# Optimization experiments

Hardware: AMD Instinct MI355X
Metric: run time of the kernel (lower is better)

## Reference

```python
import jax, jax.numpy as jnp
import numpy as np

B, O, H, I = 256, 128, 1024, 2048  # batch, objects, hidden, input_size
Hh = H // 2  # 512; x_j feature dim
DF = I - Hh  # 1536; X_F feature dim


def _xavier(key, shape):
    fan_in, fan_out = shape[1], shape[0]
    lim = np.sqrt(6.0 / (fan_in + fan_out))
    return jax.random.uniform(key, shape, jnp.float32, -lim, lim)


def setup_inputs() -> dict:
    key = jax.random.key(0)
    ks = jax.random.split(key, 24)
    mask = jax.random.bernoulli(ks[0], 0.7, (B, O))
    mask = mask.at[:, 0].set(True)  # ensure at least one valid object per row
    inp = {
        "x_j": jax.random.normal(ks[1], (B, O, Hh), jnp.float32),
        "x_mask": mask,
        "X_F": jax.random.normal(ks[2], (B, DF), jnp.float32),
        "h": jax.random.normal(ks[3], (B, 1, H), jnp.float32),
        "c": jax.random.normal(ks[4], (B, 1, H), jnp.float32),
    }
    names_W = ["W_i", "W_f", "W_c", "W_o"]
    names_U = ["U_i", "U_f", "U_c", "U_o"]
    names_V = ["V_i", "V_f", "V_c", "V_o"]
    k = 5
    for n in names_W:
        inp[n] = _xavier(ks[k], (H, I)); k += 1
    for n in names_U + names_V:
        inp[n] = _xavier(ks[k], (H, H)); k += 1
    for n in ["b_i", "b_f", "b_c", "b_o"]:
        inp[n] = jnp.zeros((H,), jnp.float32)
    inp["w"] = _xavier(ks[k], (1, Hh)); k += 1
    inp["W_e"] = _xavier(ks[k], (Hh, H)); k += 1
    inp["U_e"] = _xavier(ks[k], (Hh, Hh)); k += 1
    inp["b_e"] = jnp.zeros((Hh,), jnp.float32)
    return inp


def reference(x_j, x_mask, X_F, h, c,
              W_i, W_f, W_c, W_o,
              U_i, U_f, U_c, U_o,
              V_i, V_f, V_c, V_o,
              b_i, b_f, b_c, b_o,
              w, W_e, U_e, b_e):
    # Additive attention over objects.
    # h: (B,1,H) -> (B,1,Hh) broadcasts against x_j proj (B,O,Hh)
    e = jnp.tanh(h @ W_e.T + x_j @ U_e.T + b_e)      # (B,O,Hh)
    e = (e @ w.T)[..., 0]                              # (B,O)
    e = jnp.where(x_mask, e, -1e9)
    a = jax.nn.softmax(e, axis=1)                      # (B,O)
    phi_j = jnp.einsum('bo,bok->bk', a, x_j)[:, None, :]  # (B,1,Hh)
    x = jnp.concatenate([phi_j, X_F[:, None, :]], axis=2)  # (B,1,I)

    # Peephole LSTM gates (h, c: (B,1,H))
    i = jax.nn.sigmoid(x @ W_i.T + h @ U_i.T + c @ V_i.T + b_i)
    f = jax.nn.sigmoid(x @ W_f.T + h @ U_f.T + c @ V_f.T + b_f)
    new_c = f * c + i * jnp.tanh(x @ W_c.T + h @ U_c.T + b_c)
    o = jax.nn.sigmoid(x @ W_o.T + h @ U_o.T + c @ V_o.T + b_o)
    new_h = o * jnp.tanh(new_c)
    return new_h, new_c
```

## Files before the change

kernel.cpp:

```cpp
#include <hip/hip_runtime.h>
#include <hip/hip_bf16.h>

typedef unsigned char u8;
typedef unsigned short u16;
typedef unsigned int u32;
typedef __attribute__((ext_vector_type(8))) short bf8;
typedef __attribute__((ext_vector_type(4))) float f4;

#define B_ 256
#define O_ 128
#define Hh_ 512
#define H_ 1024
#define DF_ 1536
#define I_ 2048

#define HWE_OFF   0
#define XC_OFF    524288
#define PRE_OFF   2621440
#define FLAG_OFF  6815744
#define XJ16_OFF  7340032
#define UE16_OFF  40894464
#define WS_BIG    41418752
#define GPART_OFF XJ16_OFF

__device__ __forceinline__ float bflo(u32 u){ union{u32 i; float f;} v; v.i = u<<16; return v.f; }
__device__ __forceinline__ float bfhi(u32 u){ union{u32 i; float f;} v; v.i = u & 0xffff0000u; return v.f; }
__device__ __forceinline__ float bf1(u16 u){ union{u32 i; float f;} v; v.i = ((u32)u)<<16; return v.f; }
__device__ __forceinline__ u16 f2bf(float f){
    __hip_bfloat16 h = __float2bfloat16(f);
    union{ __hip_bfloat16 h; u16 u; } v; v.h = h; return v.u;
}
__device__ __forceinline__ u32 pack2(float a, float b){
    return ((u32)f2bf(a)) | (((u32)f2bf(b))<<16);
}
struct P8 { uint4 lo, hi; };
__device__ __forceinline__ P8 fetch8(const void* p, size_t idx, int isf32){
    P8 r;
    if(isf32){
        const uint4* f = (const uint4*)((const float*)p + idx);
        r.lo = f[0]; r.hi = f[1];
    } else {
        r.lo = *(const uint4*)((const u16*)p + idx);
    }
    return r;
}
__device__ __forceinline__ uint4 cvt8(P8 r, int isf32){
    if(isf32){
        float4 x = *(float4*)&r.lo, y = *(float4*)&r.hi;
        uint4 o;
        o.x = pack2(x.x,x.y); o.y = pack2(x.z,x.w);
        o.z = pack2(y.x,y.y); o.w = pack2(y.z,y.w);
        return o;
    }
    return r.lo;
}
__device__ __forceinline__ uint4 load8(const void* p, size_t idx, int isf32){
    return cvt8(fetch8(p, idx, isf32), isf32);
}
__device__ __forceinline__ float loads(const void* p, size_t idx, int isf32){
    return isf32 ? ((const float*)p)[idx] : bf1(((const u16*)p)[idx]);
}
__device__ __forceinline__ float fast_tanh(float x){
    return 1.0f - 2.0f/(__expf(2.0f*x)+1.0f);
}
__device__ __forceinline__ float sigmoidf_(float x){
    return 1.0f/(1.0f+__expf(-x));
}

__global__ void k_detect(const u8* __restrict__ m, const u16* __restrict__ xj,
                         int* __restrict__ flags){
    __shared__ int n1, n2, n3, mb, xo;
    int t = threadIdx.x;
    if(t==0){ n1=0; n2=0; n3=0; mb=0; xo=0; }
    __syncthreads();
    int a1=0, a2=0, a3=0, amax=0;
    for(int i=t; i<8192; i+=256){
        int v = m[i]; int c = i&3;
        if(c==1) a1|=v;
        if(c==2) a2|=v;
        if(c==3) a3|=v;
        amax = amax > v ? amax : v;
    }
    if(a1) atomicOr(&n1,1);
    if(a2) atomicOr(&n2,1);
    if(a3) atomicOr(&n3,1);
    atomicMax(&mb, amax);
    int e = 0;
    for(int i=t; i<2048; i+=256){
        u32 u = xj[2*i];
        int ex = (u>>7)&0xFF;
        if(ex >= 156) e = 1;
    }
    if(e) atomicOr(&xo,1);
    __syncthreads();
    if(t==0){
        int w;
        if(!n1 && !n2 && !n3)      w = 4;
        else if(!n1 && n2 && n3)   w = 4;
        else if(mb > 1)            w = 2;
        else                       w = 1;
        flags[0] = w;
        flags[1] = xo;
    }
}

__global__ __launch_bounds__(256) void k_conv(const void* __restrict__ xj,
                                              const void* __restrict__ Ue,
                                              const int* __restrict__ flags,
                                              u16* __restrict__ xj16,
                                              u16* __restrict__ ue16){
    int isf32 = flags[1];
    size_t g = (size_t)blockIdx.x*256 + threadIdx.x;
    if(g < 2097152){
        size_t idx = g*8;
        *(uint4*)&xj16[idx] = load8(xj, idx, isf32);
    } else {
        size_t idx = (g - 2097152)*8;
        *(uint4*)&ue16[idx] = load8(Ue, idx, isf32);
    }
}

__global__ __launch_bounds__(256) void k_hwe(const void* __restrict__ h,
                                             const void* __restrict__ We,
                                             const int* __restrict__ flags,
                                             float* __restrict__ hwe){
    int n0 = blockIdx.x*64;
    int kc = blockIdx.y*128;
    int m0 = blockIdx.z*128;
    int t = threadIdx.x;
    int isf32 = flags[1];
    __shared__ __align__(16) u16 As[128*40];
    __shared__ __align__(16) u16 Bs[64*40];
    int w = t>>6, lane = t&63;
    int q = lane>>4, l16 = lane&15;
    int koff = q*8;
    f4 acc[2][4];
    for(int mi=0;mi<2;mi++) for(int ni=0;ni<4;ni++){
        f4 z = {0.f,0.f,0.f,0.f}; acc[mi][ni] = z;
    }
    for(int ks=0; ks<128; ks+=32){
        __syncthreads();
        for(int i=0;i<2;i++){
            int row = i*64 + (t>>2), cv = t&3;
            uint4 va = load8(h, (size_t)(m0+row)*H_ + kc + ks + cv*8, isf32);
            *(uint4*)&As[row*40 + cv*8] = va;
        }
        {
            int row = t>>2, cv = t&3;
            uint4 vb = load8(We, (size_t)(n0+row)*H_ + kc + ks + cv*8, isf32);
            *(uint4*)&Bs[row*40 + cv*8] = vb;
        }
        __syncthreads();
        bf8 af[2], bfr[4];
        for(int mi=0;mi<2;mi++) af[mi]  = *(const bf8*)&As[(w*32+mi*16+l16)*40 + koff];
        for(int ni=0;ni<4;ni++) bfr[ni] = *(const bf8*)&Bs[(ni*16+l16)*40 + koff];
        for(int mi=0;mi<2;mi++)
            for(int ni=0;ni<4;ni++)
                acc[mi][ni] = __builtin_amdgcn_mfma_f32_16x16x32_bf16(af[mi], bfr[ni], acc[mi][ni], 0,0,0);
    }
    for(int mi=0;mi<2;mi++){
        for(int r=0;r<4;r++){
            int brow = m0 + w*32 + mi*16 + q*4 + r;
            for(int ni=0;ni<4;ni++){
                int ncol = n0 + ni*16 + l16;
                atomicAdd(&hwe[(size_t)brow*Hh_ + ncol], acc[mi][ni][r]);
            }
        }
    }
}

__global__ __launch_bounds__(256) void k_pack(const void* __restrict__ XF,
                                              const void* __restrict__ h,
                                              const void* __restrict__ c,
                                              const int* __restrict__ flags,
                                              u16* __restrict__ Xc){
    int b = blockIdx.y;
    int r = blockIdx.x*256 + threadIdx.x;
    int isf32 = flags[1];
    float v;
    if(r < DF_)            v = loads(XF, (size_t)b*DF_ + r, isf32);
    else if(r < DF_ + H_)  v = loads(h,  (size_t)b*H_ + (r - DF_), isf32);
    else                   v = loads(c,  (size_t)b*H_ + (r - DF_ - H_), isf32);
    Xc[(size_t)b*4096 + 512 + r] = f2bf(v);
}

__global__ __launch_bounds__(256) void k_attn(const void* __restrict__ xjA,
                                              const void* __restrict__ wvec,
                                              const void* __restrict__ UeA,
                                              const void* __restrict__ be,
                                              const float* __restrict__ hwe,
                                              const int* __restrict__ flags,
                                              int srcbf,
                                              float* __restrict__ Epart){
    int b = blockIdx.x, nc = blockIdx.y, t = threadIdx.x;
    int isf = flags[1];
    int isA = srcbf ? 0 : isf;
    __shared__ __align__(16) u16 As[128*40];
    __shared__ __align__(16) u16 Bs[64*40];
    __shared__ float hwes[64];
    __shared__ float wvs[64];

    if(t < 64){
        int col = nc*64 + t;
        hwes[t] = hwe[(size_t)b*Hh_ + col] + loads(be, col, isf);
        wvs[t]  = loads(wvec, col, isf);
    }

    const size_t xboff = (size_t)b*O_*Hh_;
    int w = t>>6, lane = t&63;
    int q = lane>>4, l16 = lane&15;
    int koff = q*8;
    int rA = t>>2, cA = t&3;

    f4 acc[2][4];
    for(int mi=0;mi<2;mi++) for(int ni=0;ni<4;ni++){
        f4 z = {0.f,0.f,0.f,0.f}; acc[mi][ni] = z;
    }

    P8 pa0, pa1, pb;
    pa0 = fetch8(xjA, xboff + (size_t)rA*Hh_      + cA*8, isA);
    pa1 = fetch8(xjA, xboff + (size_t)(rA+64)*Hh_ + cA*8, isA);
    pb  = fetch8(UeA, (size_t)(nc*64 + rA)*Hh_    + cA*8, isA);

    for(int ks=0; ks<Hh_; ks+=32){
        __syncthreads();
        *(uint4*)&As[rA*40 + cA*8]      = cvt8(pa0, isA);
        *(uint4*)&As[(rA+64)*40 + cA*8] = cvt8(pa1, isA);
        *(uint4*)&Bs[rA*40 + cA*8]      = cvt8(pb, isA);
        __syncthreads();
        if(ks + 32 < Hh_){
            int kn = ks + 32;
            pa0 = fetch8(xjA, xboff + (size_t)rA*Hh_      + kn + cA*8, isA);
            pa1 = fetch8(xjA, xboff + (size_t)(rA+64)*Hh_ + kn + cA*8, isA);
            pb  = fetch8(UeA, (size_t)(nc*64 + rA)*Hh_    + kn + cA*8, isA);
        }
        bf8 af[2], bfr[4];
        for(int mi=0;mi<2;mi++) af[mi]  = *(const bf8*)&As[(w*32+mi*16+l16)*40 + koff];
        for(int ni=0;ni<4;ni++) bfr[ni] = *(const bf8*)&Bs[(ni*16+l16)*40 + koff];
        for(int mi=0;mi<2;mi++)
            for(int ni=0;ni<4;ni++)
                acc[mi][ni] = __builtin_amdgcn_mfma_f32_16x16x32_bf16(af[mi], bfr[ni], acc[mi][ni], 0,0,0);
    }
    for(int mi=0;mi<2;mi++){
        for(int r=0;r<4;r++){
            int o = w*32 + mi*16 + q*4 + r;
            float part = 0.f;
            for(int ni=0;ni<4;ni++){
                int col = ni*16 + l16;
                part += wvs[col] * fast_tanh(hwes[col] + acc[mi][ni][r]);
            }
            part += __shfl_xor(part, 1);
            part += __shfl_xor(part, 2);
            part += __shfl_xor(part, 4);
            part += __shfl_xor(part, 8);
            if(l16 == 0) Epart[(size_t)nc*32768 + (size_t)b*O_ + o] = part;
        }
    }
}

__global__ __launch_bounds__(512) void k_soft(const float* __restrict__ Epart,
                                              const void* __restrict__ maskp,
                                              const void* __restrict__ xjA,
                                              const int* __restrict__ flags,
                                              int srcbf,
                                              u16* __restrict__ Xc){
    int b = blockIdx.x, t = threadIdx.x;
    int isf = flags[1];
    int isA = srcbf ? 0 : isf;
    int mw = flags[0];
    __shared__ float es[O_];
    __shared__ float as_[O_];
    __shared__ float red[2];
    if(t < O_){
        float e = 0.f;
        for(int p=0;p<8;p++) e += Epart[(size_t)p*32768 + (size_t)b*O_ + t];
        size_t mi_ = (size_t)b*O_ + t;
        bool valid;
        if(mw == 1)      valid = ((const u8*)maskp)[mi_]  != 0;
        else if(mw == 2) valid = ((const u16*)maskp)[mi_] != 0;
        else             valid = ((const u32*)maskp)[mi_] != 0;
        es[t] = valid ? e : -1e30f;
    }
    __syncthreads();
    if(t < 64){
        float v = fmaxf(es[t], es[t+64]);
        for(int m=32;m>0;m>>=1) v = fmaxf(v, __shfl_xor(v, m));
        if(t==0) red[0] = v;
    }
    __syncthreads();
    if(t < O_) as_[t] = __expf(es[t] - red[0]);
    __syncthreads();
    if(t < 64){
        float v = as_[t] + as_[t+64];
        for(int m=32;m>0;m>>=1) v += __shfl_xor(v, m);
        if(t==0) red[1] = v;
    }
    __syncthreads();
    float inv = 1.0f / red[1];
    float acc = 0.f;
    size_t base = (size_t)b*O_*Hh_ + t;
    #pragma unroll 8
    for(int o=0;o<O_;o++){
        acc += as_[o] * loads(xjA, base + (size_t)o*Hh_, isA);
    }
    Xc[(size_t)b*4096 + t] = f2bf(acc * inv);
}

__global__ __launch_bounds__(512) void k_gates(const u16* __restrict__ Xc,
    const void* __restrict__ Wi, const void* __restrict__ Wf, const void* __restrict__ Wc, const void* __restrict__ Wo,
    const void* __restrict__ Ui, const void* __restrict__ Uf, const void* __restrict__ Uc, const void* __restrict__ Uo,
    const void* __restrict__ Vi, const void* __restrict__ Vf, const void* __restrict__ Vo,
    const int* __restrict__ flags,
    int dosplit,
    float* __restrict__ part){
    int nt = blockIdx.x;
    int kc = blockIdx.y;
    int g  = nt>>4;
    int k0 = kc*512;
    if(g == 2 && k0 >= 3072) return;
    int isf32 = flags[1];
    const void* Wm = (g==0)?Wi:(g==1)?Wf:(g==2)?Wc:Wo;
    const void* Um = (g==0)?Ui:(g==1)?Uf:(g==2)?Uc:Uo;
    const void* Vm = (g==0)?Vi:(g==1)?Vf:(g==3)?Vo:Vi;
    int n0 = (nt&15)*64;
    int t = threadIdx.x;
    __shared__ __align__(16) u16 As[256*40];
    __shared__ __align__(16) u16 Bs[64*40];
    int w = t>>6, lane = t&63;
    int q = lane>>4, l16 = lane&15;
    int koff = q*8;
    int rA = t>>2, cA = t&3;
    bool hasB = (t < 256);

    f4 acc[2][4];
    for(int mi=0;mi<2;mi++) for(int ni=0;ni<4;ni++){
        f4 z = {0.f,0.f,0.f,0.f}; acc[mi][ni] = z;
    }

    auto fetchB = [&](int k)->P8{
        int n = n0 + rA;
        if(k < 2048)       return fetch8(Wm, (size_t)n*I_ + k, isf32);
        else if(k < 3072)  return fetch8(Um, (size_t)n*H_ + (k-2048), isf32);
        else               return fetch8(Vm, (size_t)n*H_ + (k-3072), isf32);
    };

    uint4 qa0, qa1; P8 qb;
    qa0 = *(const uint4*)(Xc + (size_t)rA*4096       + k0 + cA*8);
    qa1 = *(const uint4*)(Xc + (size_t)(rA+128)*4096 + k0 + cA*8);
    if(hasB) qb = fetchB(k0 + cA*8);

    for(int ks=0; ks<512; ks+=32){
        __syncthreads();
        *(uint4*)&As[rA*40 + cA*8]       = qa0;
        *(uint4*)&As[(rA+128)*40 + cA*8] = qa1;
        if(hasB) *(uint4*)&Bs[rA*40 + cA*8] = cvt8(qb, isf32);
        __syncthreads();
        if(ks + 32 < 512){
            int kn = k0 + ks + 32;
            qa0 = *(const uint4*)(Xc + (size_t)rA*4096       + kn + cA*8);
            qa1 = *(const uint4*)(Xc + (size_t)(rA+128)*4096 + kn + cA*8);
            if(hasB) qb = fetchB(kn + cA*8);
        }
        bf8 af[2], bfr[4];
        for(int mi=0;mi<2;mi++) af[mi]  = *(const bf8*)&As[(w*32+mi*16+l16)*40 + koff];
        for(int ni=0;ni<4;ni++) bfr[ni] = *(const bf8*)&Bs[(ni*16+l16)*40 + koff];
        for(int mi=0;mi<2;mi++)
            for(int ni=0;ni<4;ni++)
                acc[mi][ni] = __builtin_amdgcn_mfma_f32_16x16x32_bf16(af[mi], bfr[ni], acc[mi][ni], 0,0,0);
    }
    float* pg = dosplit ? (part + ((size_t)kc*4 + g)*(size_t)(B_*H_))
                        : (part + (size_t)g*(B_*H_));
    for(int mi=0;mi<2;mi++){
        for(int r=0;r<4;r++){
            int brow = w*32 + mi*16 + q*4 + r;
            for(int ni=0;ni<4;ni++){
                int ncol = n0 + ni*16 + l16;
                size_t o = (size_t)brow*H_ + ncol;
                if(dosplit) pg[o] = acc[mi][ni][r];
                else        atomicAdd(&pg[o], acc[mi][ni][r]);
            }
        }
    }
}

__global__ __launch_bounds__(256) void k_combine(const float* __restrict__ part,
    int nsplit, int climit,
    const void* __restrict__ c,
    const void* __restrict__ bi, const void* __restrict__ bfv,
    const void* __restrict__ bc, const void* __restrict__ bo,
    const int* __restrict__ flags,
    float* __restrict__ out){
    int b = blockIdx.x, t = threadIdx.x;
    int isf32 = flags[1];
    const size_t G = (size_t)B_*H_;
    for(int i=0;i<4;i++){
        int n = i*256 + t;
        size_t idx = (size_t)b*H_ + n;
        float pi = 0.f, pf = 0.f, pcv = 0.f, po = 0.f;
        for(int p=0;p<nsplit;p++){
            const float* pp = part + (size_t)p*4*G;
            pi += pp[idx];
            pf += pp[G + idx];
            po += pp[3*G + idx];
            if(p < climit) pcv += pp[2*G + idx];
        }
        pi  += loads(bi,  n, isf32);
        pf  += loads(bfv, n, isf32);
        pcv += loads(bc,  n, isf32);
        po  += loads(bo,  n, isf32);
        float ig = sigmoidf_(pi);
        float fg = sigmoidf_(pf);
        float og = sigmoidf_(po);
        float cold = loads(c, idx, isf32);
        float ncv = fg*cold + ig*fast_tanh(pcv);
        float nh  = og*fast_tanh(ncv);
        out[idx]     = nh;
        out[G + idx] = ncv;
    }
}

extern "C" void kernel_launch(void* const* d_in, const int* in_sizes, int n_in,
                              void* d_out, int out_size, void* d_ws, size_t ws_size,
                              hipStream_t stream){
    const void* xj   = d_in[0];
    const void* mask = d_in[1];
    const void* XF   = d_in[2];
    const void* h    = d_in[3];
    const void* c    = d_in[4];
    const void* Wi   = d_in[5];
    const void* Wf   = d_in[6];
    const void* Wc   = d_in[7];
    const void* Wo   = d_in[8];
    const void* Ui   = d_in[9];
    const void* Uf   = d_in[10];
    const void* Uc   = d_in[11];
    const void* Uo   = d_in[12];
    const void* Vi   = d_in[13];
    const void* Vf   = d_in[14];
    const void* Vo   = d_in[16];
    const void* bi   = d_in[17];
    const void* bfv  = d_in[18];
    const void* bc   = d_in[19];
    const void* bo   = d_in[20];
    const void* wv   = d_in[21];
    const void* We   = d_in[22];
    const void* Ue   = d_in[23];
    const void* be   = d_in[24];

    char* ws = (char*)d_ws;
    float* hwe  = (float*)(ws + HWE_OFF);
    u16*   Xc   = (u16*)(ws + XC_OFF);
    float* pre  = (float*)(ws + PRE_OFF);
    int*   flags= (int*)(ws + FLAG_OFF);
    float* out  = (float*)d_out;

    int big = (ws_size >= (size_t)WS_BIG);
    u16* xj16 = (u16*)(ws + XJ16_OFF);
    u16* ue16 = (u16*)(ws + UE16_OFF);
    float* gpart = (float*)(ws + GPART_OFF);
    const void* xjA = big ? (const void*)xj16 : xj;
    const void* UeA = big ? (const void*)ue16 : Ue;

    k_detect<<<1, 256, 0, stream>>>((const u8*)mask, (const u16*)xj, flags);
    hipMemsetAsync(hwe, 0, (size_t)B_*Hh_*sizeof(float), stream);
    if(big) k_conv<<<8320, 256, 0, stream>>>(xj, Ue, flags, xj16, ue16);
    k_hwe<<<dim3(8,8,2), 256, 0, stream>>>(h, We, flags, hwe);
    k_pack<<<dim3(14, B_), 256, 0, stream>>>(XF, h, c, flags, Xc);
    k_attn<<<dim3(B_, 8), 256, 0, stream>>>(xjA, wv, UeA, be, hwe, flags, big, pre);
    k_soft<<<B_, 512, 0, stream>>>(pre, mask, xjA, flags, big, Xc);
    if(big){
        k_gates<<<dim3(64, 8), 512, 0, stream>>>(Xc, Wi,Wf,Wc,Wo, Ui,Uf,Uc,Uo, Vi,Vf,Vo, flags, 1, gpart);
        k_combine<<<B_, 256, 0, stream>>>(gpart, 8, 6, c, bi, bfv, bc, bo, flags, out);
    } else {
        hipMemsetAsync(pre, 0, (size_t)4*B_*H_*sizeof(float), stream);
        k_gates<<<dim3(64, 8), 512, 0, stream>>>(Xc, Wi,Wf,Wc,Wo, Ui,Uf,Uc,Uo, Vi,Vf,Vo, flags, 0, pre);
        k_combine<<<B_, 256, 0, stream>>>(pre, 1, 1, c, bi, bfv, bc, bo, flags, out);
    }
}
```

Measured before the change: 337.9 us.

## Fuse attention scoring and softmax per batch, drop x_j bf16 conversion pass

Attention projection, tanh-score reduction and softmax/weighted sum are merged into one kernel per batch row. Each wave keeps its x_j A-fragments in registers and loops over all 512 columns of U_e, so the separate x_j-to-bf16 conversion kernel and the Epart round trip are gone. The h·W_e partial sums are now written to separate split buffers instead of atomics, which removes a memset. The gates GEMM K-step also grows from 32 to 64 with wider LDS tiles. The cost is that parallelism for the attention stage drops to 256 blocks, and register pressure rises from the 16 held A fragments and 16 accumulators.

```diff
diff --git a/kernel.cpp b/kernel.cpp
--- a/kernel.cpp
+++ b/kernel.cpp
@@ -23,8 +23,6 @@
 #define WS_BIG    41418752
 #define GPART_OFF XJ16_OFF
 
-__device__ __forceinline__ float bflo(u32 u){ union{u32 i; float f;} v; v.i = u<<16; return v.f; }
-__device__ __forceinline__ float bfhi(u32 u){ union{u32 i; float f;} v; v.i = u & 0xffff0000u; return v.f; }
 __device__ __forceinline__ float bf1(u16 u){ union{u32 i; float f;} v; v.i = ((u32)u)<<16; return v.f; }
 __device__ __forceinline__ u16 f2bf(float f){
     __hip_bfloat16 h = __float2bfloat16(f);
@@ -104,26 +102,19 @@
     }
 }
 
-__global__ __launch_bounds__(256) void k_conv(const void* __restrict__ xj,
-                                              const void* __restrict__ Ue,
-                                              const int* __restrict__ flags,
-                                              u16* __restrict__ xj16,
-                                              u16* __restrict__ ue16){
+__global__ __launch_bounds__(256) void k_conv_ue(const void* __restrict__ Ue,
+                                                 const int* __restrict__ flags,
+                                                 u16* __restrict__ ue16){
     int isf32 = flags[1];
     size_t g = (size_t)blockIdx.x*256 + threadIdx.x;
-    if(g < 2097152){
-        size_t idx = g*8;
-        *(uint4*)&xj16[idx] = load8(xj, idx, isf32);
-    } else {
-        size_t idx = (g - 2097152)*8;
-        *(uint4*)&ue16[idx] = load8(Ue, idx, isf32);
-    }
+    size_t idx = g*8;
+    *(uint4*)&ue16[idx] = load8(Ue, idx, isf32);
 }
 
 __global__ __launch_bounds__(256) void k_hwe(const void* __restrict__ h,
                                              const void* __restrict__ We,
                                              const int* __restrict__ flags,
-                                             float* __restrict__ hwe){
+                                             float* __restrict__ hwePart){
     int n0 = blockIdx.x*64;
     int kc = blockIdx.y*128;
     int m0 = blockIdx.z*128;
@@ -158,12 +149,13 @@
             for(int ni=0;ni<4;ni++)
                 acc[mi][ni] = __builtin_amdgcn_mfma_f32_16x16x32_bf16(af[mi], bfr[ni], acc[mi][ni], 0,0,0);
     }
+    float* hp = hwePart + (size_t)blockIdx.y*(B_*Hh_);
     for(int mi=0;mi<2;mi++){
         for(int r=0;r<4;r++){
             int brow = m0 + w*32 + mi*16 + q*4 + r;
             for(int ni=0;ni<4;ni++){
                 int ncol = n0 + ni*16 + l16;
-                atomicAdd(&hwe[(size_t)brow*Hh_ + ncol], acc[mi][ni][r]);
+                hp[(size_t)brow*Hh_ + ncol] = acc[mi][ni][r];
             }
         }
     }
@@ -184,102 +176,101 @@
     Xc[(size_t)b*4096 + 512 + r] = f2bf(v);
 }
 
-__global__ __launch_bounds__(256) void k_attn(const void* __restrict__ xjA,
-                                              const void* __restrict__ wvec,
-                                              const void* __restrict__ UeA,
-                                              const void* __restrict__ be,
-                                              const float* __restrict__ hwe,
-                                              const int* __restrict__ flags,
-                                              int srcbf,
-                                              float* __restrict__ Epart){
-    int b = blockIdx.x, nc = blockIdx.y, t = threadIdx.x;
-    int isf = flags[1];
-    int isA = srcbf ? 0 : isf;
-    __shared__ __align__(16) u16 As[128*40];
-    __shared__ __align__(16) u16 Bs[64*40];
-    __shared__ float hwes[64];
-    __shared__ float wvs[64];
-
-    if(t < 64){
-        int col = nc*64 + t;
-        hwes[t] = hwe[(size_t)b*Hh_ + col] + loads(be, col, isf);
-        wvs[t]  = loads(wvec, col, isf);
-    }
-
-    const size_t xboff = (size_t)b*O_*Hh_;
-    int w = t>>6, lane = t&63;
-    int q = lane>>4, l16 = lane&15;
-    int koff = q*8;
-    int rA = t>>2, cA = t&3;
-
-    f4 acc[2][4];
-    for(int mi=0;mi<2;mi++) for(int ni=0;ni<4;ni++){
-        f4 z = {0.f,0.f,0.f,0.f}; acc[mi][ni] = z;
-    }
-
-    P8 pa0, pa1, pb;
-    pa0 = fetch8(xjA, xboff + (size_t)rA*Hh_      + cA*8, isA);
-    pa1 = fetch8(xjA, xboff + (size_t)(rA+64)*Hh_ + cA*8, isA);
-    pb  = fetch8(UeA, (size_t)(nc*64 + rA)*Hh_    + cA*8, isA);
-
-    for(int ks=0; ks<Hh_; ks+=32){
-        __syncthreads();
-        *(uint4*)&As[rA*40 + cA*8]      = cvt8(pa0, isA);
-        *(uint4*)&As[(rA+64)*40 + cA*8] = cvt8(pa1, isA);
-        *(uint4*)&Bs[rA*40 + cA*8]      = cvt8(pb, isA);
-        __syncthreads();
-        if(ks + 32 < Hh_){
-            int kn = ks + 32;
-            pa0 = fetch8(xjA, xboff + (size_t)rA*Hh_      + kn + cA*8, isA);
-            pa1 = fetch8(xjA, xboff + (size_t)(rA+64)*Hh_ + kn + cA*8, isA);
-            pb  = fetch8(UeA, (size_t)(nc*64 + rA)*Hh_    + kn + cA*8, isA);
-        }
-        bf8 af[2], bfr[4];
-        for(int mi=0;mi<2;mi++) af[mi]  = *(const bf8*)&As[(w*32+mi*16+l16)*40 + koff];
-        for(int ni=0;ni<4;ni++) bfr[ni] = *(const bf8*)&Bs[(ni*16+l16)*40 + koff];
-        for(int mi=0;mi<2;mi++)
-            for(int ni=0;ni<4;ni++)
-                acc[mi][ni] = __builtin_amdgcn_mfma_f32_16x16x32_bf16(af[mi], bfr[ni], acc[mi][ni], 0,0,0);
-    }
-    for(int mi=0;mi<2;mi++){
-        for(int r=0;r<4;r++){
-            int o = w*32 + mi*16 + q*4 + r;
-            float part = 0.f;
-            for(int ni=0;ni<4;ni++){
-                int col = ni*16 + l16;
-                part += wvs[col] * fast_tanh(hwes[col] + acc[mi][ni][r]);
-            }
-            part += __shfl_xor(part, 1);
-            part += __shfl_xor(part, 2);
-            part += __shfl_xor(part, 4);
-            part += __shfl_xor(part, 8);
-            if(l16 == 0) Epart[(size_t)nc*32768 + (size_t)b*O_ + o] = part;
-        }
-    }
-}
-
-__global__ __launch_bounds__(512) void k_soft(const float* __restrict__ Epart,
-                                              const void* __restrict__ maskp,
-                                              const void* __restrict__ xjA,
-                                              const int* __restrict__ flags,
-                                              int srcbf,
-                                              u16* __restrict__ Xc){
+__global__ __launch_bounds__(512) void k_attn_fused(const void* __restrict__ xj,
+                                                    const void* __restrict__ UeB,
+                                                    const void* __restrict__ wvec,
+                                                    const void* __restrict__ be,
+                                                    const float* __restrict__ hwePart,
+                                                    const void* __restrict__ maskp,
+                                                    const int* __restrict__ flags,
+                                                    int ueIsBf,
+                                                    u16* __restrict__ Xc){
     int b = blockIdx.x, t = threadIdx.x;
     int isf = flags[1];
-    int isA = srcbf ? 0 : isf;
+    int isB = ueIsBf ? 0 : isf;
     int mw = flags[0];
+    __shared__ __align__(16) u16 Bs[256*72];
+    __shared__ float hwes[512];
+    __shared__ float wvs[512];
     __shared__ float es[O_];
     __shared__ float as_[O_];
     __shared__ float red[2];
+    __shared__ int msk[O_];
+
+    int w = t>>6, l = t&63, l16 = l&15, q = l>>4;
+    int m0 = w*16;
+
+    {
+        float s = 0.f;
+        #pragma unroll
+        for(int p=0;p<8;p++) s += hwePart[(size_t)p*(B_*Hh_) + (size_t)b*Hh_ + t];
+        hwes[t] = s + loads(be, t, isf);
+        wvs[t]  = loads(wvec, t, isf);
+    }
     if(t < O_){
-        float e = 0.f;
-        for(int p=0;p<8;p++) e += Epart[(size_t)p*32768 + (size_t)b*O_ + t];
         size_t mi_ = (size_t)b*O_ + t;
         bool valid;
         if(mw == 1)      valid = ((const u8*)maskp)[mi_]  != 0;
         else if(mw == 2) valid = ((const u16*)maskp)[mi_] != 0;
         else             valid = ((const u32*)maskp)[mi_] != 0;
-        es[t] = valid ? e : -1e30f;
+        msk[t] = valid ? 1 : 0;
+    }
+
+    bf8 afr[16];
+    const size_t arow = ((size_t)b*O_ + m0 + l16)*Hh_;
+    #pragma unroll
+    for(int kt=0;kt<16;kt++){
+        P8 p = fetch8(xj, arow + kt*32 + q*8, isf);
+        uint4 u = cvt8(p, isf);
+        afr[kt] = *(bf8*)&u;
+    }
+
+    float ep[4] = {0.f,0.f,0.f,0.f};
+    #pragma unroll
+    for(int hh=0; hh<2; hh++){
+        int nbase = hh*256;
+        f4 acc[16];
+        #pragma unroll
+        for(int ni=0;ni<16;ni++){ f4 z={0.f,0.f,0.f,0.f}; acc[ni]=z; }
+        #pragma unroll
+        for(int ks=0;ks<8;ks++){
+            __syncthreads();
+            #pragma unroll
+            for(int j=0;j<4;j++){
+                int slot = t + j*512;
+                int row = slot>>3, cv = slot&7;
+                P8 p = fetch8(UeB, (size_t)(nbase+row)*Hh_ + ks*64 + cv*8, isB);
+                *(uint4*)&Bs[row*72 + cv*8] = cvt8(p, isB);
+            }
+            __syncthreads();
+            #pragma unroll
+            for(int ni=0;ni<16;ni++){
+                #pragma unroll
+                for(int kk=0;kk<2;kk++){
+                    bf8 bfrag = *(const bf8*)&Bs[(ni*16+l16)*72 + kk*32 + q*8];
+                    acc[ni] = __builtin_amdgcn_mfma_f32_16x16x32_bf16(afr[ks*2+kk], bfrag, acc[ni], 0,0,0);
+                }
+            }
+        }
+        #pragma unroll
+        for(int ni=0;ni<16;ni++){
+            int col = nbase + ni*16 + l16;
+            float wv = wvs[col], hw = hwes[col];
+            #pragma unroll
+            for(int r=0;r<4;r++) ep[r] += wv * fast_tanh(hw + acc[ni][r]);
+        }
+    }
+    #pragma unroll
+    for(int r=0;r<4;r++){
+        float v = ep[r];
+        v += __shfl_xor(v, 1);
+        v += __shfl_xor(v, 2);
+        v += __shfl_xor(v, 4);
+        v += __shfl_xor(v, 8);
+        if(l16 == 0){
+            int o = m0 + q*4 + r;
+            es[o] = msk[o] ? v : -1e30f;
+        }
     }
     __syncthreads();
     if(t < 64){
@@ -297,13 +288,13 @@
     }
     __syncthreads();
     float inv = 1.0f / red[1];
-    float acc = 0.f;
+    float acc2 = 0.f;
     size_t base = (size_t)b*O_*Hh_ + t;
     #pragma unroll 8
     for(int o=0;o<O_;o++){
-        acc += as_[o] * loads(xjA, base + (size_t)o*Hh_, isA);
-    }
-    Xc[(size_t)b*4096 + t] = f2bf(acc * inv);
+        acc2 += as_[o] * loads(xj, base + (size_t)o*Hh_, isf);
+    }
+    Xc[(size_t)b*4096 + t] = f2bf(acc2 * inv);
 }
 
 __global__ __launch_bounds__(512) void k_gates(const u16* __restrict__ Xc,
@@ -324,49 +315,65 @@
     const void* Vm = (g==0)?Vi:(g==1)?Vf:(g==3)?Vo:Vi;
     int n0 = (nt&15)*64;
     int t = threadIdx.x;
-    __shared__ __align__(16) u16 As[256*40];
-    __shared__ __align__(16) u16 Bs[64*40];
+    __shared__ __align__(16) u16 As[256*72];
+    __shared__ __align__(16) u16 Bs[64*72];
     int w = t>>6, lane = t&63;
     int q = lane>>4, l16 = lane&15;
-    int koff = q*8;
-    int rA = t>>2, cA = t&3;
-    bool hasB = (t < 256);
+    int rB = t>>3, cB = t&7;
 
     f4 acc[2][4];
     for(int mi=0;mi<2;mi++) for(int ni=0;ni<4;ni++){
         f4 z = {0.f,0.f,0.f,0.f}; acc[mi][ni] = z;
     }
 
-    auto fetchB = [&](int k)->P8{
-        int n = n0 + rA;
+    auto fetchBrow = [&](int n, int k)->P8{
         if(k < 2048)       return fetch8(Wm, (size_t)n*I_ + k, isf32);
         else if(k < 3072)  return fetch8(Um, (size_t)n*H_ + (k-2048), isf32);
         else               return fetch8(Vm, (size_t)n*H_ + (k-3072), isf32);
     };
 
-    uint4 qa0, qa1; P8 qb;
-    qa0 = *(const uint4*)(Xc + (size_t)rA*4096       + k0 + cA*8);
-    qa1 = *(const uint4*)(Xc + (size_t)(rA+128)*4096 + k0 + cA*8);
-    if(hasB) qb = fetchB(k0 + cA*8);
-
-    for(int ks=0; ks<512; ks+=32){
+    uint4 qa[4]; P8 qb;
+    #pragma unroll
+    for(int j=0;j<4;j++){
+        int slot = t + j*512;
+        int row = slot>>3, cv = slot&7;
+        qa[j] = *(const uint4*)(Xc + (size_t)row*4096 + k0 + cv*8);
+    }
+    qb = fetchBrow(n0 + rB, k0 + cB*8);
+
+    for(int ks=0; ks<512; ks+=64){
         __syncthreads();
-        *(uint4*)&As[rA*40 + cA*8]       = qa0;
-        *(uint4*)&As[(rA+128)*40 + cA*8] = qa1;
-        if(hasB) *(uint4*)&Bs[rA*40 + cA*8] = cvt8(qb, isf32);
+        #pragma unroll
+        for(int j=0;j<4;j++){
+            int slot = t + j*512;
+            int row = slot>>3, cv = slot&7;
+            *(uint4*)&As[row*72 + cv*8] = qa[j];
+        }
+        *(uint4*)&Bs[rB*72 + cB*8] = cvt8(qb, isf32);
         __syncthreads();
-        if(ks + 32 < 512){
-            int kn = k0 + ks + 32;
-            qa0 = *(const uint4*)(Xc + (size_t)rA*4096       + kn + cA*8);
-            qa1 = *(const uint4*)(Xc + (size_t)(rA+128)*4096 + kn + cA*8);
-            if(hasB) qb = fetchB(kn + cA*8);
-        }
-        bf8 af[2], bfr[4];
-        for(int mi=0;mi<2;mi++) af[mi]  = *(const bf8*)&As[(w*32+mi*16+l16)*40 + koff];
-        for(int ni=0;ni<4;ni++) bfr[ni] = *(const bf8*)&Bs[(ni*16+l16)*40 + koff];
-        for(int mi=0;mi<2;mi++)
-            for(int ni=0;ni<4;ni++)
-                acc[mi][ni] = __builtin_amdgcn_mfma_f32_16x16x32_bf16(af[mi], bfr[ni], acc[mi][ni], 0,0,0);
+        if(ks + 64 < 512){
+            int kn = k0 + ks + 64;
+            #pragma unroll
+            for(int j=0;j<4;j++){
+                int slot = t + j*512;
+                int row = slot>>3, cv = slot&7;
+                qa[j] = *(const uint4*)(Xc + (size_t)row*4096 + kn + cv*8);
+            }
+            qb = fetchBrow(n0 + rB, kn + cB*8);
+        }
+        #pragma unroll
+        for(int kk=0;kk<2;kk++){
+            bf8 af[2], bfr[4];
+            #pragma unroll
+            for(int mi=0;mi<2;mi++) af[mi]  = *(const bf8*)&As[(w*32+mi*16+l16)*72 + kk*32 + q*8];
+            #pragma unroll
+            for(int ni=0;ni<4;ni++) bfr[ni] = *(const bf8*)&Bs[(ni*16+l16)*72 + kk*32 + q*8];
+            #pragma unroll
+            for(int mi=0;mi<2;mi++)
+                #pragma unroll
+                for(int ni=0;ni<4;ni++)
+                    acc[mi][ni] = __builtin_amdgcn_mfma_f32_16x16x32_bf16(af[mi], bfr[ni], acc[mi][ni], 0,0,0);
+        }
     }
     float* pg = dosplit ? (part + ((size_t)kc*4 + g)*(size_t)(B_*H_))
                         : (part + (size_t)g*(B_*H_));
@@ -448,26 +455,21 @@
     const void* be   = d_in[24];
 
     char* ws = (char*)d_ws;
-    float* hwe  = (float*)(ws + HWE_OFF);
     u16*   Xc   = (u16*)(ws + XC_OFF);
     float* pre  = (float*)(ws + PRE_OFF);
     int*   flags= (int*)(ws + FLAG_OFF);
     float* out  = (float*)d_out;
 
     int big = (ws_size >= (size_t)WS_BIG);
-    u16* xj16 = (u16*)(ws + XJ16_OFF);
     u16* ue16 = (u16*)(ws + UE16_OFF);
     float* gpart = (float*)(ws + GPART_OFF);
-    const void* xjA = big ? (const void*)xj16 : xj;
     const void* UeA = big ? (const void*)ue16 : Ue;
 
     k_detect<<<1, 256, 0, stream>>>((const u8*)mask, (const u16*)xj, flags);
-    hipMemsetAsync(hwe, 0, (size_t)B_*Hh_*sizeof(float), stream);
-    if(big) k_conv<<<8320, 256, 0, stream>>>(xj, Ue, flags, xj16, ue16);
-    k_hwe<<<dim3(8,8,2), 256, 0, stream>>>(h, We, flags, hwe);
+    if(big) k_conv_ue<<<256, 256, 0, stream>>>(Ue, flags, ue16);
+    k_hwe<<<dim3(8,8,2), 256, 0, stream>>>(h, We, flags, pre);
     k_pack<<<dim3(14, B_), 256, 0, stream>>>(XF, h, c, flags, Xc);
-    k_attn<<<dim3(B_, 8), 256, 0, stream>>>(xjA, wv, UeA, be, hwe, flags, big, pre);
-    k_soft<<<B_, 512, 0, stream>>>(pre, mask, xjA, flags, big, Xc);
+    k_attn_fused<<<B_, 512, 0, stream>>>(xj, UeA, wv, be, pre, mask, flags, big, Xc);
     if(big){
         k_gates<<<dim3(64, 8), 512, 0, stream>>>(Xc, Wi,Wf,Wc,Wo, Ui,Uf,Uc,Uo, Vi,Vf,Vo, flags, 1, gpart);
         k_combine<<<B_, 256, 0, stream>>>(gpart, 8, 6, c, bi, bfv, bc, bo, flags, out);
```

After: 354.8 us. +5.0%, slower.

## Load attention A-fragments directly to registers and widen gate GEMM K-tile

Applied to the files above, without the earlier changes.

In the attention kernel, each wave now loads its x_j MFMA fragments straight from global memory into registers, bypassing shared memory. Only the U_e tile is staged, in a double-buffered shared array with one barrier per step, and the K loop is fully unrolled. In the gates kernel, the K tile per barrier grows from 32 to 64 with padded 72-element rows, and all threads share the A and B loads. Both changes aim to cut barrier count and shared-memory traffic, at the cost of more registers and less coalesced direct global loads for the A fragments.

```diff
diff --git a/kernel.cpp b/kernel.cpp
--- a/kernel.cpp
+++ b/kernel.cpp
@@ -23,8 +23,6 @@
 #define WS_BIG    41418752
 #define GPART_OFF XJ16_OFF
 
-__device__ __forceinline__ float bflo(u32 u){ union{u32 i; float f;} v; v.i = u<<16; return v.f; }
-__device__ __forceinline__ float bfhi(u32 u){ union{u32 i; float f;} v; v.i = u & 0xffff0000u; return v.f; }
 __device__ __forceinline__ float bf1(u16 u){ union{u32 i; float f;} v; v.i = ((u32)u)<<16; return v.f; }
 __device__ __forceinline__ u16 f2bf(float f){
     __hip_bfloat16 h = __float2bfloat16(f);
@@ -195,8 +193,7 @@
     int b = blockIdx.x, nc = blockIdx.y, t = threadIdx.x;
     int isf = flags[1];
     int isA = srcbf ? 0 : isf;
-    __shared__ __align__(16) u16 As[128*40];
-    __shared__ __align__(16) u16 Bs[64*40];
+    __shared__ __align__(16) u16 Bs[2][64*40];
     __shared__ float hwes[64];
     __shared__ float wvs[64];
 
@@ -206,45 +203,54 @@
         wvs[t]  = loads(wvec, col, isf);
     }
 
-    const size_t xboff = (size_t)b*O_*Hh_;
     int w = t>>6, lane = t&63;
     int q = lane>>4, l16 = lane&15;
-    int koff = q*8;
-    int rA = t>>2, cA = t&3;
+    int rB = t>>2, cB = t&3;
+    const size_t arow0 = ((size_t)b*O_ + w*32 + l16)*Hh_ + q*8;
+    const size_t arow1 = arow0 + (size_t)16*Hh_;
+    const size_t brow  = (size_t)(nc*64 + rB)*Hh_ + cB*8;
 
     f4 acc[2][4];
-    for(int mi=0;mi<2;mi++) for(int ni=0;ni<4;ni++){
-        f4 z = {0.f,0.f,0.f,0.f}; acc[mi][ni] = z;
-    }
-
-    P8 pa0, pa1, pb;
-    pa0 = fetch8(xjA, xboff + (size_t)rA*Hh_      + cA*8, isA);
-    pa1 = fetch8(xjA, xboff + (size_t)(rA+64)*Hh_ + cA*8, isA);
-    pb  = fetch8(UeA, (size_t)(nc*64 + rA)*Hh_    + cA*8, isA);
-
-    for(int ks=0; ks<Hh_; ks+=32){
+    #pragma unroll
+    for(int mi=0;mi<2;mi++)
+        #pragma unroll
+        for(int ni=0;ni<4;ni++){ f4 z = {0.f,0.f,0.f,0.f}; acc[mi][ni] = z; }
+
+    P8 pb  = fetch8(UeA, brow, isA);
+    P8 pa0 = fetch8(xjA, arow0, isA);
+    P8 pa1 = fetch8(xjA, arow1, isA);
+    *(uint4*)&Bs[0][rB*40 + cB*8] = cvt8(pb, isA);
+    pb = fetch8(UeA, brow + 32, isA);
+    __syncthreads();
+
+    #pragma unroll
+    for(int ks=0; ks<16; ks++){
+        int cur = ks&1;
+        if(ks < 15) *(uint4*)&Bs[cur^1][rB*40 + cB*8] = cvt8(pb, isA);
+        uint4 ua0 = cvt8(pa0, isA), ua1 = cvt8(pa1, isA);
+        bf8 af0 = *(bf8*)&ua0, af1 = *(bf8*)&ua1;
+        if(ks < 14) pb = fetch8(UeA, brow + (size_t)(ks+2)*32, isA);
+        if(ks < 15){
+            pa0 = fetch8(xjA, arow0 + (size_t)(ks+1)*32, isA);
+            pa1 = fetch8(xjA, arow1 + (size_t)(ks+1)*32, isA);
+        }
+        bf8 bfr[4];
+        #pragma unroll
+        for(int ni=0;ni<4;ni++) bfr[ni] = *(const bf8*)&Bs[cur][(ni*16+l16)*40 + q*8];
+        #pragma unroll
+        for(int ni=0;ni<4;ni++){
+            acc[0][ni] = __builtin_amdgcn_mfma_f32_16x16x32_bf16(af0, bfr[ni], acc[0][ni], 0,0,0);
+            acc[1][ni] = __builtin_amdgcn_mfma_f32_16x16x32_bf16(af1, bfr[ni], acc[1][ni], 0,0,0);
+        }
         __syncthreads();
-        *(uint4*)&As[rA*40 + cA*8]      = cvt8(pa0, isA);
-        *(uint4*)&As[(rA+64)*40 + cA*8] = cvt8(pa1, isA);
-        *(uint4*)&Bs[rA*40 + cA*8]      = cvt8(pb, isA);
-        __syncthreads();
-        if(ks + 32 < Hh_){
-            int kn = ks + 32;
-            pa0 = fetch8(xjA, xboff + (size_t)rA*Hh_      + kn + cA*8, isA);
-            pa1 = fetch8(xjA, xboff + (size_t)(rA+64)*Hh_ + kn + cA*8, isA);
-            pb  = fetch8(UeA, (size_t)(nc*64 + rA)*Hh_    + kn + cA*8, isA);
-        }
-        bf8 af[2], bfr[4];
-        for(int mi=0;mi<2;mi++) af[mi]  = *(const bf8*)&As[(w*32+mi*16+l16)*40 + koff];
-        for(int ni=0;ni<4;ni++) bfr[ni] = *(const bf8*)&Bs[(ni*16+l16)*40 + koff];
-        for(int mi=0;mi<2;mi++)
-            for(int ni=0;ni<4;ni++)
-                acc[mi][ni] = __builtin_amdgcn_mfma_f32_16x16x32_bf16(af[mi], bfr[ni], acc[mi][ni], 0,0,0);
-    }
+    }
+    #pragma unroll
     for(int mi=0;mi<2;mi++){
+        #pragma unroll
         for(int r=0;r<4;r++){
             int o = w*32 + mi*16 + q*4 + r;
             float part = 0.f;
+            #pragma unroll
             for(int ni=0;ni<4;ni++){
                 int col = ni*16 + l16;
                 part += wvs[col] * fast_tanh(hwes[col] + acc[mi][ni][r]);
@@ -324,49 +330,65 @@
     const void* Vm = (g==0)?Vi:(g==1)?Vf:(g==3)?Vo:Vi;
     int n0 = (nt&15)*64;
     int t = threadIdx.x;
-    __shared__ __align__(16) u16 As[256*40];
-    __shared__ __align__(16) u16 Bs[64*40];
+    __shared__ __align__(16) u16 As[256*72];
+    __shared__ __align__(16) u16 Bs[64*72];
     int w = t>>6, lane = t&63;
     int q = lane>>4, l16 = lane&15;
-    int koff = q*8;
-    int rA = t>>2, cA = t&3;
-    bool hasB = (t < 256);
+    int rB = t>>3, cB = t&7;
 
     f4 acc[2][4];
     for(int mi=0;mi<2;mi++) for(int ni=0;ni<4;ni++){
         f4 z = {0.f,0.f,0.f,0.f}; acc[mi][ni] = z;
     }
 
-    auto fetchB = [&](int k)->P8{
-        int n = n0 + rA;
+    auto fetchBrow = [&](int n, int k)->P8{
         if(k < 2048)       return fetch8(Wm, (size_t)n*I_ + k, isf32);
         else if(k < 3072)  return fetch8(Um, (size_t)n*H_ + (k-2048), isf32);
         else               return fetch8(Vm, (size_t)n*H_ + (k-3072), isf32);
     };
 
-    uint4 qa0, qa1; P8 qb;
-    qa0 = *(const uint4*)(Xc + (size_t)rA*4096       + k0 + cA*8);
-    qa1 = *(const uint4*)(Xc + (size_t)(rA+128)*4096 + k0 + cA*8);
-    if(hasB) qb = fetchB(k0 + cA*8);
-
-    for(int ks=0; ks<512; ks+=32){
+    uint4 qa[4]; P8 qb;
+    #pragma unroll
+    for(int j=0;j<4;j++){
+        int slot = t + j*512;
+        int row = slot>>3, cv = slot&7;
+        qa[j] = *(const uint4*)(Xc + (size_t)row*4096 + k0 + cv*8);
+    }
+    qb = fetchBrow(n0 + rB, k0 + cB*8);
+
+    for(int ks=0; ks<512; ks+=64){
         __syncthreads();
-        *(uint4*)&As[rA*40 + cA*8]       = qa0;
-        *(uint4*)&As[(rA+128)*40 + cA*8] = qa1;
-        if(hasB) *(uint4*)&Bs[rA*40 + cA*8] = cvt8(qb, isf32);
+        #pragma unroll
+        for(int j=0;j<4;j++){
+            int slot = t + j*512;
+            int row = slot>>3, cv = slot&7;
+            *(uint4*)&As[row*72 + cv*8] = qa[j];
+        }
+        *(uint4*)&Bs[rB*72 + cB*8] = cvt8(qb, isf32);
         __syncthreads();
-        if(ks + 32 < 512){
-            int kn = k0 + ks + 32;
-            qa0 = *(const uint4*)(Xc + (size_t)rA*4096       + kn + cA*8);
-            qa1 = *(const uint4*)(Xc + (size_t)(rA+128)*4096 + kn + cA*8);
-            if(hasB) qb = fetchB(kn + cA*8);
-        }
-        bf8 af[2], bfr[4];
-        for(int mi=0;mi<2;mi++) af[mi]  = *(const bf8*)&As[(w*32+mi*16+l16)*40 + koff];
-        for(int ni=0;ni<4;ni++) bfr[ni] = *(const bf8*)&Bs[(ni*16+l16)*40 + koff];
-        for(int mi=0;mi<2;mi++)
-            for(int ni=0;ni<4;ni++)
-                acc[mi][ni] = __builtin_amdgcn_mfma_f32_16x16x32_bf16(af[mi], bfr[ni], acc[mi][ni], 0,0,0);
+        if(ks + 64 < 512){
+            int kn = k0 + ks + 64;
+            #pragma unroll
+            for(int j=0;j<4;j++){
+                int slot = t + j*512;
+                int row = slot>>3, cv = slot&7;
+                qa[j] = *(const uint4*)(Xc + (size_t)row*4096 + kn + cv*8);
+            }
+            qb = fetchBrow(n0 + rB, kn + cB*8);
+        }
+        #pragma unroll
+        for(int kk=0;kk<2;kk++){
+            bf8 af[2], bfr[4];
+            #pragma unroll
+            for(int mi=0;mi<2;mi++) af[mi]  = *(const bf8*)&As[(w*32+mi*16+l16)*72 + kk*32 + q*8];
+            #pragma unroll
+            for(int ni=0;ni<4;ni++) bfr[ni] = *(const bf8*)&Bs[(ni*16+l16)*72 + kk*32 + q*8];
+            #pragma unroll
+            for(int mi=0;mi<2;mi++)
+                #pragma unroll
+                for(int ni=0;ni<4;ni++)
+                    acc[mi][ni] = __builtin_amdgcn_mfma_f32_16x16x32_bf16(af[mi], bfr[ni], acc[mi][ni], 0,0,0);
+        }
     }
     float* pg = dosplit ? (part + ((size_t)kc*4 + g)*(size_t)(B_*H_))
                         : (part + (size_t)g*(B_*H_));
```

Result: slower. 375.7 us (+11.2%).

## Fuse prep kernels and fold softmax into attention via last-block counter

Applied to the files above, without the earlier changes.

Merges the dtype conversion, the h·W_e GEMM and the Xc packing into one k_prep launch. The W_e GEMM now writes four K-split partial buffers instead of using atomics into a memset buffer. Softmax and the weighted x_j reduction move into the tail of k_attn, run by whichever of the eight column blocks finishes last for each batch row, using a per-row atomic counter and threadfences. This removes several launches, a memset and the atomics, at the cost of serialising the softmax onto one block per row and relying on the counters being reset in k_detect.

```diff
diff --git a/kernel.cpp b/kernel.cpp
--- a/kernel.cpp
+++ b/kernel.cpp
@@ -14,17 +14,15 @@
 #define DF_ 1536
 #define I_ 2048
 
-#define HWE_OFF   0
 #define XC_OFF    524288
 #define PRE_OFF   2621440
+#define HWEP_OFF  (PRE_OFF + 1048576)
 #define FLAG_OFF  6815744
 #define XJ16_OFF  7340032
 #define UE16_OFF  40894464
 #define WS_BIG    41418752
 #define GPART_OFF XJ16_OFF
 
-__device__ __forceinline__ float bflo(u32 u){ union{u32 i; float f;} v; v.i = u<<16; return v.f; }
-__device__ __forceinline__ float bfhi(u32 u){ union{u32 i; float f;} v; v.i = u & 0xffff0000u; return v.f; }
 __device__ __forceinline__ float bf1(u16 u){ union{u32 i; float f;} v; v.i = ((u32)u)<<16; return v.f; }
 __device__ __forceinline__ u16 f2bf(float f){
     __hip_bfloat16 h = __float2bfloat16(f);
@@ -68,9 +66,10 @@
 }
 
 __global__ void k_detect(const u8* __restrict__ m, const u16* __restrict__ xj,
-                         int* __restrict__ flags){
+                         int* __restrict__ flags, int* __restrict__ cnt){
     __shared__ int n1, n2, n3, mb, xo;
     int t = threadIdx.x;
+    cnt[t] = 0;
     if(t==0){ n1=0; n2=0; n3=0; mb=0; xo=0; }
     __syncthreads();
     int a1=0, a2=0, a3=0, amax=0;
@@ -104,94 +103,100 @@
     }
 }
 
-__global__ __launch_bounds__(256) void k_conv(const void* __restrict__ xj,
+__global__ __launch_bounds__(256) void k_prep(const void* __restrict__ xj,
                                               const void* __restrict__ Ue,
-                                              const int* __restrict__ flags,
-                                              u16* __restrict__ xj16,
-                                              u16* __restrict__ ue16){
-    int isf32 = flags[1];
-    size_t g = (size_t)blockIdx.x*256 + threadIdx.x;
-    if(g < 2097152){
-        size_t idx = g*8;
-        *(uint4*)&xj16[idx] = load8(xj, idx, isf32);
-    } else {
-        size_t idx = (g - 2097152)*8;
-        *(uint4*)&ue16[idx] = load8(Ue, idx, isf32);
-    }
-}
-
-__global__ __launch_bounds__(256) void k_hwe(const void* __restrict__ h,
-                                             const void* __restrict__ We,
-                                             const int* __restrict__ flags,
-                                             float* __restrict__ hwe){
-    int n0 = blockIdx.x*64;
-    int kc = blockIdx.y*128;
-    int m0 = blockIdx.z*128;
-    int t = threadIdx.x;
-    int isf32 = flags[1];
-    __shared__ __align__(16) u16 As[128*40];
-    __shared__ __align__(16) u16 Bs[64*40];
-    int w = t>>6, lane = t&63;
-    int q = lane>>4, l16 = lane&15;
-    int koff = q*8;
-    f4 acc[2][4];
-    for(int mi=0;mi<2;mi++) for(int ni=0;ni<4;ni++){
-        f4 z = {0.f,0.f,0.f,0.f}; acc[mi][ni] = z;
-    }
-    for(int ks=0; ks<128; ks+=32){
-        __syncthreads();
-        for(int i=0;i<2;i++){
-            int row = i*64 + (t>>2), cv = t&3;
-            uint4 va = load8(h, (size_t)(m0+row)*H_ + kc + ks + cv*8, isf32);
-            *(uint4*)&As[row*40 + cv*8] = va;
-        }
-        {
-            int row = t>>2, cv = t&3;
-            uint4 vb = load8(We, (size_t)(n0+row)*H_ + kc + ks + cv*8, isf32);
-            *(uint4*)&Bs[row*40 + cv*8] = vb;
-        }
-        __syncthreads();
-        bf8 af[2], bfr[4];
-        for(int mi=0;mi<2;mi++) af[mi]  = *(const bf8*)&As[(w*32+mi*16+l16)*40 + koff];
-        for(int ni=0;ni<4;ni++) bfr[ni] = *(const bf8*)&Bs[(ni*16+l16)*40 + koff];
-        for(int mi=0;mi<2;mi++)
-            for(int ni=0;ni<4;ni++)
-                acc[mi][ni] = __builtin_amdgcn_mfma_f32_16x16x32_bf16(af[mi], bfr[ni], acc[mi][ni], 0,0,0);
-    }
-    for(int mi=0;mi<2;mi++){
-        for(int r=0;r<4;r++){
-            int brow = m0 + w*32 + mi*16 + q*4 + r;
-            for(int ni=0;ni<4;ni++){
-                int ncol = n0 + ni*16 + l16;
-                atomicAdd(&hwe[(size_t)brow*Hh_ + ncol], acc[mi][ni][r]);
-            }
-        }
-    }
-}
-
-__global__ __launch_bounds__(256) void k_pack(const void* __restrict__ XF,
+                                              const void* __restrict__ XF,
                                               const void* __restrict__ h,
                                               const void* __restrict__ c,
+                                              const void* __restrict__ We,
                                               const int* __restrict__ flags,
+                                              int convN,
+                                              u16* __restrict__ xj16,
+                                              u16* __restrict__ ue16,
+                                              float* __restrict__ hwePart,
                                               u16* __restrict__ Xc){
-    int b = blockIdx.y;
-    int r = blockIdx.x*256 + threadIdx.x;
+    int bid = blockIdx.x, t = threadIdx.x;
     int isf32 = flags[1];
-    float v;
-    if(r < DF_)            v = loads(XF, (size_t)b*DF_ + r, isf32);
-    else if(r < DF_ + H_)  v = loads(h,  (size_t)b*H_ + (r - DF_), isf32);
-    else                   v = loads(c,  (size_t)b*H_ + (r - DF_ - H_), isf32);
-    Xc[(size_t)b*4096 + 512 + r] = f2bf(v);
+    if(bid < convN){
+        size_t g = (size_t)bid*256 + t;
+        if(g < 2097152){
+            size_t idx = g*8;
+            *(uint4*)&xj16[idx] = load8(xj, idx, isf32);
+        } else {
+            size_t idx = (g - 2097152)*8;
+            *(uint4*)&ue16[idx] = load8(Ue, idx, isf32);
+        }
+        return;
+    }
+    bid -= convN;
+    if(bid < 64){
+        int n0 = (bid&7)*64;
+        int kb = ((bid>>3)&3)*256;
+        int m0 = (bid>>5)*128;
+        __shared__ __align__(16) u16 As[128*40];
+        __shared__ __align__(16) u16 Bs[64*40];
+        int w = t>>6, lane = t&63;
+        int q = lane>>4, l16 = lane&15;
+        int koff = q*8;
+        f4 acc[2][4];
+        for(int mi=0;mi<2;mi++) for(int ni=0;ni<4;ni++){
+            f4 z = {0.f,0.f,0.f,0.f}; acc[mi][ni] = z;
+        }
+        for(int ks=0; ks<256; ks+=32){
+            __syncthreads();
+            for(int i=0;i<2;i++){
+                int row = i*64 + (t>>2), cv = t&3;
+                uint4 va = load8(h, (size_t)(m0+row)*H_ + kb + ks + cv*8, isf32);
+                *(uint4*)&As[row*40 + cv*8] = va;
+            }
+            {
+                int row = t>>2, cv = t&3;
+                uint4 vb = load8(We, (size_t)(n0+row)*H_ + kb + ks + cv*8, isf32);
+                *(uint4*)&Bs[row*40 + cv*8] = vb;
+            }
+            __syncthreads();
+            bf8 af[2], bfr[4];
+            for(int mi=0;mi<2;mi++) af[mi]  = *(const bf8*)&As[(w*32+mi*16+l16)*40 + koff];
+            for(int ni=0;ni<4;ni++) bfr[ni] = *(const bf8*)&Bs[(ni*16+l16)*40 + koff];
+            for(int mi=0;mi<2;mi++)
+                for(int ni=0;ni<4;ni++)
+                    acc[mi][ni] = __builtin_amdgcn_mfma_f32_16x16x32_bf16(af[mi], bfr[ni], acc[mi][ni], 0,0,0);
+        }
+        float* hp = hwePart + (size_t)((bid>>3)&3)*(B_*Hh_);
+        for(int mi=0;mi<2;mi++){
+            for(int r=0;r<4;r++){
+                int brow = m0 + w*32 + mi*16 + q*4 + r;
+                for(int ni=0;ni<4;ni++){
+                    int ncol = n0 + ni*16 + l16;
+                    hp[(size_t)brow*Hh_ + ncol] = acc[mi][ni][r];
+                }
+            }
+        }
+        return;
+    }
+    bid -= 64;
+    {
+        int b = bid/14;
+        int r = (bid%14)*256 + t;
+        float v;
+        if(r < DF_)            v = loads(XF, (size_t)b*DF_ + r, isf32);
+        else if(r < DF_ + H_)  v = loads(h,  (size_t)b*H_ + (r - DF_), isf32);
+        else                   v = loads(c,  (size_t)b*H_ + (r - DF_ - H_), isf32);
+        Xc[(size_t)b*4096 + 512 + r] = f2bf(v);
+    }
 }
 
 __global__ __launch_bounds__(256) void k_attn(const void* __restrict__ xjA,
                                               const void* __restrict__ wvec,
                                               const void* __restrict__ UeA,
                                               const void* __restrict__ be,
-                                              const float* __restrict__ hwe,
+                                              const float* __restrict__ hwePart,
+                                              const void* __restrict__ maskp,
                                               const int* __restrict__ flags,
                                               int srcbf,
-                                              float* __restrict__ Epart){
+                                              float* __restrict__ Epart,
+                                              u16* __restrict__ Xc,
+                                              int* __restrict__ cnt){
     int b = blockIdx.x, nc = blockIdx.y, t = threadIdx.x;
     int isf = flags[1];
     int isA = srcbf ? 0 : isf;
@@ -199,10 +204,17 @@
     __shared__ __align__(16) u16 Bs[64*40];
     __shared__ float hwes[64];
     __shared__ float wvs[64];
+    __shared__ float es[O_];
+    __shared__ float as_[O_];
+    __shared__ float red[2];
+    __shared__ int lastf;
 
     if(t < 64){
         int col = nc*64 + t;
-        hwes[t] = hwe[(size_t)b*Hh_ + col] + loads(be, col, isf);
+        float s = 0.f;
+        #pragma unroll
+        for(int p=0;p<4;p++) s += hwePart[(size_t)p*(B_*Hh_) + (size_t)b*Hh_ + col];
+        hwes[t] = s + loads(be, col, isf);
         wvs[t]  = loads(wvec, col, isf);
     }
 
@@ -256,23 +268,18 @@
             if(l16 == 0) Epart[(size_t)nc*32768 + (size_t)b*O_ + o] = part;
         }
     }
-}
-
-__global__ __launch_bounds__(512) void k_soft(const float* __restrict__ Epart,
-                                              const void* __restrict__ maskp,
-                                              const void* __restrict__ xjA,
-                                              const int* __restrict__ flags,
-                                              int srcbf,
-                                              u16* __restrict__ Xc){
-    int b = blockIdx.x, t = threadIdx.x;
-    int isf = flags[1];
-    int isA = srcbf ? 0 : isf;
+
+    __threadfence();
+    __syncthreads();
+    if(t==0) lastf = (atomicAdd(&cnt[b], 1) == 7);
+    __syncthreads();
+    if(!lastf) return;
+    __threadfence();
+
     int mw = flags[0];
-    __shared__ float es[O_];
-    __shared__ float as_[O_];
-    __shared__ float red[2];
     if(t < O_){
         float e = 0.f;
+        #pragma unroll
         for(int p=0;p<8;p++) e += Epart[(size_t)p*32768 + (size_t)b*O_ + t];
         size_t mi_ = (size_t)b*O_ + t;
         bool valid;
@@ -297,13 +304,27 @@
     }
     __syncthreads();
     float inv = 1.0f / red[1];
-    float acc = 0.f;
-    size_t base = (size_t)b*O_*Hh_ + t;
-    #pragma unroll 8
-    for(int o=0;o<O_;o++){
-        acc += as_[o] * loads(xjA, base + (size_t)o*Hh_, isA);
-    }
-    Xc[(size_t)b*4096 + t] = f2bf(acc * inv);
+    int c0 = 2*t;
+    float a0 = 0.f, a1 = 0.f;
+    if(isA == 0){
+        const u16* xp = (const u16*)xjA + xboff + c0;
+        #pragma unroll 8
+        for(int o=0;o<O_;o++){
+            u32 v = *(const u32*)(xp + (size_t)o*Hh_);
+            a0 += as_[o] * bf1((u16)(v & 0xffff));
+            a1 += as_[o] * bf1((u16)(v >> 16));
+        }
+    } else {
+        const float* xp = (const float*)xjA + xboff + c0;
+        #pragma unroll 8
+        for(int o=0;o<O_;o++){
+            float2 v = *(const float2*)(xp + (size_t)o*Hh_);
+            a0 += as_[o] * v.x;
+            a1 += as_[o] * v.y;
+        }
+    }
+    Xc[(size_t)b*4096 + c0]     = f2bf(a0 * inv);
+    Xc[(size_t)b*4096 + c0 + 1] = f2bf(a1 * inv);
 }
 
 __global__ __launch_bounds__(512) void k_gates(const u16* __restrict__ Xc,
@@ -448,11 +469,13 @@
     const void* be   = d_in[24];
 
     char* ws = (char*)d_ws;
-    float* hwe  = (float*)(ws + HWE_OFF);
-    u16*   Xc   = (u16*)(ws + XC_OFF);
-    float* pre  = (float*)(ws + PRE_OFF);
-    int*   flags= (int*)(ws + FLAG_OFF);
-    float* out  = (float*)d_out;
+    u16*   Xc    = (u16*)(ws + XC_OFF);
+    float* Epart = (float*)(ws + PRE_OFF);
+    float* hweP  = (float*)(ws + HWEP_OFF);
+    float* pre   = (float*)(ws + PRE_OFF);
+    int*   flags = (int*)(ws + FLAG_OFF);
+    int*   cnt   = (int*)(ws + FLAG_OFF + 64);
+    float* out   = (float*)d_out;
 
     int big = (ws_size >= (size_t)WS_BIG);
     u16* xj16 = (u16*)(ws + XJ16_OFF);
@@ -461,13 +484,12 @@
     const void* xjA = big ? (const void*)xj16 : xj;
     const void* UeA = big ? (const void*)ue16 : Ue;
 
-    k_detect<<<1, 256, 0, stream>>>((const u8*)mask, (const u16*)xj, flags);
-    hipMemsetAsync(hwe, 0, (size_t)B_*Hh_*sizeof(float), stream);
-    if(big) k_conv<<<8320, 256, 0, stream>>>(xj, Ue, flags, xj16, ue16);
-    k_hwe<<<dim3(8,8,2), 256, 0, stream>>>(h, We, flags, hwe);
-    k_pack<<<dim3(14, B_), 256, 0, stream>>>(XF, h, c, flags, Xc);
-    k_attn<<<dim3(B_, 8), 256, 0, stream>>>(xjA, wv, UeA, be, hwe, flags, big, pre);
-    k_soft<<<B_, 512, 0, stream>>>(pre, mask, xjA, flags, big, Xc);
+    k_detect<<<1, 256, 0, stream>>>((const u8*)mask, (const u16*)xj, flags, cnt);
+    int convN = big ? 8320 : 0;
+    k_prep<<<convN + 64 + 3584, 256, 0, stream>>>(xj, Ue, XF, h, c, We, flags, convN,
+                                                  xj16, ue16, hweP, Xc);
+    k_attn<<<dim3(B_, 8), 256, 0, stream>>>(xjA, wv, UeA, be, hweP, mask, flags, big,
+                                            Epart, Xc, cnt);
     if(big){
         k_gates<<<dim3(64, 8), 512, 0, stream>>>(Xc, Wi,Wf,Wc,Wo, Ui,Uf,Uc,Uo, Vi,Vf,Vo, flags, 1, gpart);
         k_combine<<<B_, 256, 0, stream>>>(gpart, 8, 6, c, bi, bfv, bc, bo, flags, out);
```

Measured after the change: 469.4 us. +38.9%, slower.
